# Kernel optimization log

Hardware: AMD Instinct MI355X
Metric: run time of the kernel (lower is better)

Reference implementation:

```python
import jax, jax.numpy as jnp
import numpy as np

DIM_V = 1024
NUM_HEADS = 64            # per the module arg name; actually the per-chunk size
DIM_SPLIT = DIM_V // NUM_HEADS  # 16 = effective number of attention heads (module quirk)
N_Q, N_K = 2048, 2048
DIM_Q, DIM_K = 1024, 1024


def setup_inputs() -> dict:
    key = jax.random.key(0)
    ks = jax.random.split(key, 10)
    s = 0.02
    return {
        "Q": jax.random.normal(ks[0], (N_Q, DIM_Q), dtype=jnp.float32),
        "K": jax.random.normal(ks[1], (N_K, DIM_K), dtype=jnp.float32),
        "Wq": jax.random.normal(ks[2], (DIM_V, DIM_Q), dtype=jnp.float32) * s,
        "bq": jax.random.normal(ks[3], (DIM_V,), dtype=jnp.float32) * s,
        "Wk": jax.random.normal(ks[4], (DIM_V, DIM_K), dtype=jnp.float32) * s,
        "bk": jax.random.normal(ks[5], (DIM_V,), dtype=jnp.float32) * s,
        "Wv": jax.random.normal(ks[6], (DIM_V, DIM_K), dtype=jnp.float32) * s,
        "bv": jax.random.normal(ks[7], (DIM_V,), dtype=jnp.float32) * s,
        "Wo": jax.random.normal(ks[8], (DIM_V, DIM_V), dtype=jnp.float32) * s,
        "bo": jax.random.normal(ks[9], (DIM_V,), dtype=jnp.float32) * s,
    }


def _split_heads(x):
    # jnp.split(x[None], DIM_SPLIT, axis=2) then concat on axis 0 ==
    # [DIM_SPLIT, n, NUM_HEADS] with chunk h = x[:, h*NUM_HEADS:(h+1)*NUM_HEADS]
    n = x.shape[0]
    return x.reshape(n, DIM_SPLIT, NUM_HEADS).transpose(1, 0, 2)


def reference(Q, K, Wq, bq, Wk, bk, Wv, bv, Wo, bo):
    q = Q @ Wq.T + bq            # [n_q, dim_V]
    k = K @ Wk.T + bk            # [n_k, dim_V]
    v = K @ Wv.T + bv            # [n_k, dim_V]
    Q_ = _split_heads(q)         # [H, n_q, d] with H=DIM_SPLIT, d=NUM_HEADS
    K_ = _split_heads(k)
    V_ = _split_heads(v)
    # Faithful to source: softmax first, THEN divide by sqrt(dim_V)
    A = jax.nn.softmax(jnp.einsum('hqd,hkd->hqk', Q_, K_), axis=-1)
    A = A / jnp.sqrt(jnp.float32(DIM_V))
    O = (Q_ + jnp.einsum('hqk,hkd->hqd', A, V_)).reshape(-1, DIM_V)  # [n_q, dim_V]
    # res1 = identity (ln=False)
    O = O + jax.nn.relu(O @ Wo.T + bo)
    # res2 = identity (ln=False)
    return O
```

## Files before the change

### kernel.cpp

```cpp
#include <hip/hip_runtime.h>
#include <hip/hip_bf16.h>
#include <cstdint>

typedef unsigned short u16;
typedef __attribute__((ext_vector_type(8))) short short8;
typedef __attribute__((ext_vector_type(4))) float f32x4;

__device__ __forceinline__ u16 f2b(float f) {
  uint32_t u = __float_as_uint(f);
  u += 0x7fffu + ((u >> 16) & 1u);
  return (u16)(u >> 16);
}
__device__ __forceinline__ float b2f(u16 b) {
  return __uint_as_float(((uint32_t)b) << 16);
}
__device__ __forceinline__ uint32_t pk2bf(float a, float b) {
  __hip_bfloat162 t = __float22bfloat162_rn(make_float2(a, b));
  return *(uint32_t*)&t;
}

__global__ __launch_bounds__(256) void cast_all(
    const float* __restrict__ Q, const float* __restrict__ K,
    const float* __restrict__ Wq, const float* __restrict__ Wk,
    const float* __restrict__ Wv, const float* __restrict__ Wo,
    u16* __restrict__ xq, u16* __restrict__ xk,
    u16* __restrict__ wq, u16* __restrict__ wk,
    u16* __restrict__ wv, u16* __restrict__ wo) {
  int g = blockIdx.x * 256 + threadIdx.x;
  const float* src; u16* dst; int off;
  if      (g <  524288) { src = Q;  dst = xq; off = g; }
  else if (g < 1048576) { src = K;  dst = xk; off = g -  524288; }
  else if (g < 1310720) { src = Wq; dst = wq; off = g - 1048576; }
  else if (g < 1572864) { src = Wk; dst = wk; off = g - 1310720; }
  else if (g < 1835008) { src = Wv; dst = wv; off = g - 1572864; }
  else                  { src = Wo; dst = wo; off = g - 1835008; }
  float4 v = reinterpret_cast<const float4*>(src)[off];
  ushort4 o4;
  o4.x = f2b(v.x); o4.y = f2b(v.y); o4.z = f2b(v.z); o4.w = f2b(v.w);
  reinterpret_cast<ushort4*>(dst)[off] = o4;
}

__global__ __launch_bounds__(256) void gemm3(
    const u16* __restrict__ xq, const u16* __restrict__ xk,
    const u16* __restrict__ wq, const u16* __restrict__ wk,
    const u16* __restrict__ wv,
    const float* __restrict__ bq, const float* __restrict__ bk,
    const float* __restrict__ bv,
    u16* __restrict__ qb, u16* __restrict__ kb, u16* __restrict__ vT) {
  __shared__ __align__(16) u16 sA[128 * 40];
  __shared__ __align__(16) u16 sB[64 * 40];
  const int t = threadIdx.x, blk = blockIdx.x, z = blockIdx.y;
  const int xcd = blk & 7, lid = blk >> 3;
  const u16 *A, *B; const float* bias; u16* C; int ldC, mbase, nbase; bool brow;
  if (z == 0)      { A = xq; B = wq; bias = bq; C = qb; ldC = 1024;
                     mbase = (xcd * 2 + (lid >> 4)) * 128; nbase = (lid & 15) * 64; brow = false; }
  else if (z == 1) { A = xk; B = wk; bias = bk; C = kb; ldC = 1024;
                     mbase = (xcd * 2 + (lid >> 4)) * 128; nbase = (lid & 15) * 64; brow = false; }
  else             { A = wv; B = xk; bias = bv; C = vT; ldC = 2048;
                     mbase = xcd * 128; nbase = lid * 64; brow = true; }
  const int lane = t & 63, wid = t >> 6;
  const int wy = wid >> 1, wx = wid & 1;
  const int m = lane & 15, quad = lane >> 4;

  const int arow = t >> 1, acb = (t & 1) * 16;
  const int brow_ = t >> 2, bcb = (t & 3) * 8;
  const u16* gA = A + (mbase + arow) * 1024 + acb;
  const u16* gB = B + (nbase + brow_) * 1024 + bcb;

  uint4 ra0 = *(const uint4*)(gA);
  uint4 ra1 = *(const uint4*)(gA + 8);
  uint4 rb0 = *(const uint4*)(gB);

  f32x4 acc[4][2];
#pragma unroll
  for (int i = 0; i < 4; i++)
#pragma unroll
    for (int j = 0; j < 2; j++) acc[i][j] = (f32x4){0.f, 0.f, 0.f, 0.f};

  for (int kb_ = 0; kb_ < 32; ++kb_) {
    __syncthreads();
    *(uint4*)(&sA[arow * 40 + acb])     = ra0;
    *(uint4*)(&sA[arow * 40 + acb + 8]) = ra1;
    *(uint4*)(&sB[brow_ * 40 + bcb])    = rb0;
    if (kb_ < 31) {
      ra0 = *(const uint4*)(gA + (kb_ + 1) * 32);
      ra1 = *(const uint4*)(gA + (kb_ + 1) * 32 + 8);
      rb0 = *(const uint4*)(gB + (kb_ + 1) * 32);
    }
    __syncthreads();
    short8 af[4], bf[2];
#pragma unroll
    for (int mi = 0; mi < 4; mi++)
      af[mi] = *(const short8*)(&sA[(wy * 64 + mi * 16 + m) * 40 + quad * 8]);
#pragma unroll
    for (int ni = 0; ni < 2; ni++)
      bf[ni] = *(const short8*)(&sB[(wx * 32 + ni * 16 + m) * 40 + quad * 8]);
#pragma unroll
    for (int mi = 0; mi < 4; mi++)
#pragma unroll
      for (int ni = 0; ni < 2; ni++)
        acc[mi][ni] = __builtin_amdgcn_mfma_f32_16x16x32_bf16(
            af[mi], bf[ni], acc[mi][ni], 0, 0, 0);
  }

#pragma unroll
  for (int mi = 0; mi < 4; mi++)
#pragma unroll
    for (int ni = 0; ni < 2; ni++) {
      const int col = nbase + wx * 32 + ni * 16 + m;
      const float bcol = brow ? 0.f : bias[col];
#pragma unroll
      for (int r = 0; r < 4; r++) {
        const int row = mbase + wy * 64 + mi * 16 + quad * 4 + r;
        const float bval = brow ? bias[row] : bcol;
        C[row * ldC + col] = f2b(acc[mi][ni][r] + bval);
      }
    }
}

__global__ __launch_bounds__(256) void gemm_out(
    const u16* __restrict__ A, const u16* __restrict__ B,
    const float* __restrict__ bias, const u16* __restrict__ Res,
    float* __restrict__ out) {
  __shared__ __align__(16) u16 sA[64 * 40];
  __shared__ __align__(16) u16 sB[64 * 40];
  const int t = threadIdx.x, blk = blockIdx.x;
  const int xcd = blk & 7, lid = blk >> 3;
  const int mbase = (xcd * 4 + (lid >> 4)) * 64, nbase = (lid & 15) * 64;
  const int lane = t & 63, wid = t >> 6;
  const int wy = wid >> 1, wx = wid & 1;
  const int m = lane & 15, quad = lane >> 4;
  const int srow = t >> 2, scb = (t & 3) * 8;
  const u16* gA = A + (mbase + srow) * 1024 + scb;
  const u16* gB = B + (nbase + srow) * 1024 + scb;
  uint4 ra = *(const uint4*)gA;
  uint4 rb = *(const uint4*)gB;

  f32x4 acc[2][2];
#pragma unroll
  for (int i = 0; i < 2; i++)
#pragma unroll
    for (int j = 0; j < 2; j++) acc[i][j] = (f32x4){0.f, 0.f, 0.f, 0.f};

  for (int kb_ = 0; kb_ < 32; ++kb_) {
    __syncthreads();
    *(uint4*)(&sA[srow * 40 + scb]) = ra;
    *(uint4*)(&sB[srow * 40 + scb]) = rb;
    if (kb_ < 31) {
      ra = *(const uint4*)(gA + (kb_ + 1) * 32);
      rb = *(const uint4*)(gB + (kb_ + 1) * 32);
    }
    __syncthreads();
    short8 af[2], bf[2];
#pragma unroll
    for (int mi = 0; mi < 2; mi++)
      af[mi] = *(const short8*)(&sA[(wy * 32 + mi * 16 + m) * 40 + quad * 8]);
#pragma unroll
    for (int ni = 0; ni < 2; ni++)
      bf[ni] = *(const short8*)(&sB[(wx * 32 + ni * 16 + m) * 40 + quad * 8]);
#pragma unroll
    for (int mi = 0; mi < 2; mi++)
#pragma unroll
      for (int ni = 0; ni < 2; ni++)
        acc[mi][ni] = __builtin_amdgcn_mfma_f32_16x16x32_bf16(
            af[mi], bf[ni], acc[mi][ni], 0, 0, 0);
  }

#pragma unroll
  for (int mi = 0; mi < 2; mi++)
#pragma unroll
    for (int ni = 0; ni < 2; ni++) {
      const int col = nbase + wx * 32 + ni * 16 + m;
      const float bcol = bias[col];
#pragma unroll
      for (int r = 0; r < 4; r++) {
        const int row = mbase + wy * 32 + mi * 16 + quad * 4 + r;
        out[row * 1024 + col] =
            b2f(Res[row * 1024 + col]) + fmaxf(acc[mi][ni][r] + bcol, 0.f);
      }
    }
}

__global__ __launch_bounds__(256, 2) void flash(
    const u16* __restrict__ q, const u16* __restrict__ k,
    const u16* __restrict__ vT, u16* __restrict__ po, float* __restrict__ lp) {
  __shared__ __align__(16) u16 sK[64 * 72];
  __shared__ __align__(16) u16 sV[64 * 72];
  __shared__ __align__(16) u16 sP[4 * 64 * 72];
  const int t = threadIdx.x;
  const int qt = blockIdx.x, h = blockIdx.y, sp = blockIdx.z;
  const int lane = t & 63, wid = t >> 6;
  const int m = lane & 15, quad = lane >> 4;
  const int colbase = h * 64;
  const int pbase = wid * 4608;
  const int kbase = sp * 512;
  const int qwave = qt * 256 + wid * 64;

  short8 aq[4][2];
#pragma unroll
  for (int mi = 0; mi < 4; mi++)
#pragma unroll
    for (int g = 0; g < 2; g++)
      aq[mi][g] = *(const short8*)(
          &q[(qwave + mi * 16 + m) * 1024 + colbase + g * 32 + quad * 8]);

  f32x4 o[4][4];
  float lpart[4] = {0.f, 0.f, 0.f, 0.f};
#pragma unroll
  for (int mi = 0; mi < 4; mi++)
#pragma unroll
    for (int nt = 0; nt < 4; nt++) o[mi][nt] = (f32x4){0.f, 0.f, 0.f, 0.f};

  const int srow = t >> 2, scb = (t & 3) * 16;
  const u16* gK = k + (kbase + srow) * 1024 + colbase + scb;
  const u16* gV = vT + (colbase + srow) * 2048 + kbase + scb;

  uint4 rk0 = *(const uint4*)(gK), rk1 = *(const uint4*)(gK + 8);
  uint4 rv0 = *(const uint4*)(gV), rv1 = *(const uint4*)(gV + 8);

  uint32_t* sP32 = (uint32_t*)sP;

  for (int kt = 0; kt < 8; ++kt) {
    __syncthreads();
    *(uint4*)(&sK[srow * 72 + scb])     = rk0;
    *(uint4*)(&sK[srow * 72 + scb + 8]) = rk1;
    *(uint4*)(&sV[srow * 72 + scb])     = rv0;
    *(uint4*)(&sV[srow * 72 + scb + 8]) = rv1;
    if (kt < 7) {
      rk0 = *(const uint4*)(gK + (kt + 1) * 65536);
      rk1 = *(const uint4*)(gK + (kt + 1) * 65536 + 8);
      rv0 = *(const uint4*)(gV + (kt + 1) * 64);
      rv1 = *(const uint4*)(gV + (kt + 1) * 64 + 8);
    }
    __syncthreads();

#pragma unroll
    for (int nt = 0; nt < 4; nt++) {
      short8 bk0 = *(const short8*)(&sK[(nt * 16 + m) * 72 + quad * 8]);
      short8 bk1 = *(const short8*)(&sK[(nt * 16 + m) * 72 + 32 + quad * 8]);
#pragma unroll
      for (int mi = 0; mi < 4; mi++) {
        f32x4 st = (f32x4){0.f, 0.f, 0.f, 0.f};
        st = __builtin_amdgcn_mfma_f32_16x16x32_bf16(bk0, aq[mi][0], st, 0, 0, 0);
        st = __builtin_amdgcn_mfma_f32_16x16x32_bf16(bk1, aq[mi][1], st, 0, 0, 0);
        float p0 = __expf(st[0] - 16.0f);
        float p1 = __expf(st[1] - 16.0f);
        float p2 = __expf(st[2] - 16.0f);
        float p3 = __expf(st[3] - 16.0f);
        lpart[mi] += (p0 + p1) + (p2 + p3);
        const int pa_ = pbase + (mi * 16 + m) * 72 + nt * 16 + quad * 4;
        sP32[pa_ >> 1]       = pk2bf(p0, p1);
        sP32[(pa_ >> 1) + 1] = pk2bf(p2, p3);
      }
    }

    short8 pa[4][2];
#pragma unroll
    for (int mi = 0; mi < 4; mi++)
#pragma unroll
      for (int g = 0; g < 2; g++)
        pa[mi][g] = *(const short8*)(&sP[pbase + (mi * 16 + m) * 72 + g * 32 + quad * 8]);
#pragma unroll
    for (int nt = 0; nt < 4; nt++) {
      short8 bv0 = *(const short8*)(&sV[(nt * 16 + m) * 72 + quad * 8]);
      short8 bv1 = *(const short8*)(&sV[(nt * 16 + m) * 72 + 32 + quad * 8]);
#pragma unroll
      for (int mi = 0; mi < 4; mi++) {
        o[mi][nt] = __builtin_amdgcn_mfma_f32_16x16x32_bf16(pa[mi][0], bv0, o[mi][nt], 0, 0, 0);
        o[mi][nt] = __builtin_amdgcn_mfma_f32_16x16x32_bf16(pa[mi][1], bv1, o[mi][nt], 0, 0, 0);
      }
    }
  }

#pragma unroll
  for (int mi = 0; mi < 4; mi++) {
    float l = lpart[mi];
    l += __shfl_xor(l, 16);
    l += __shfl_xor(l, 32);
    if (quad == 0)
      lp[(sp * 16 + h) * 2048 + qwave + mi * 16 + m] = l;
  }

#pragma unroll
  for (int mi = 0; mi < 4; mi++)
#pragma unroll
    for (int r = 0; r < 4; r++) {
      const int qg = qwave + mi * 16 + quad * 4 + r;
      const int base = ((sp * 16 + h) * 2048 + qg) * 64;
#pragma unroll
      for (int nt = 0; nt < 4; nt++)
        po[base + nt * 16 + m] = f2b(o[mi][nt][r]);
    }
}

__global__ __launch_bounds__(256) void combine(
    const u16* __restrict__ po, const float* __restrict__ lp,
    const u16* __restrict__ qb, u16* __restrict__ ob) {
  const int idx = blockIdx.x * 256 + threadIdx.x;
  const int dq = idx & 15, qg = (idx >> 4) & 2047, h = idx >> 15;
  float acc0 = 0.f, acc1 = 0.f, acc2 = 0.f, acc3 = 0.f, l = 0.f;
#pragma unroll
  for (int s = 0; s < 4; s++) {
    const ushort4 p4 = *(const ushort4*)&po[(((s * 16 + h) * 2048 + qg) * 64) + dq * 4];
    acc0 += b2f(p4.x); acc1 += b2f(p4.y); acc2 += b2f(p4.z); acc3 += b2f(p4.w);
    l += lp[(s * 16 + h) * 2048 + qg];
  }
  const float inv = 1.0f / (l * 32.0f);
  const ushort4 q4 = *(const ushort4*)&qb[qg * 1024 + h * 64 + dq * 4];
  ushort4 o4;
  o4.x = f2b(b2f(q4.x) + acc0 * inv);
  o4.y = f2b(b2f(q4.y) + acc1 * inv);
  o4.z = f2b(b2f(q4.z) + acc2 * inv);
  o4.w = f2b(b2f(q4.w) + acc3 * inv);
  *(ushort4*)&ob[(h * 128 + (qg >> 4)) * 1024 + (qg & 15) * 64 + dq * 4] = o4;
}

extern "C" void kernel_launch(void* const* d_in, const int* in_sizes, int n_in,
                              void* d_out, int out_size, void* d_ws, size_t ws_size,
                              hipStream_t stream) {
  const float* Q  = (const float*)d_in[0];
  const float* K  = (const float*)d_in[1];
  const float* Wq = (const float*)d_in[2];
  const float* bq = (const float*)d_in[3];
  const float* Wk = (const float*)d_in[4];
  const float* bk = (const float*)d_in[5];
  const float* Wv = (const float*)d_in[6];
  const float* bv = (const float*)d_in[7];
  const float* Wo = (const float*)d_in[8];
  const float* bo = (const float*)d_in[9];
  float* out = (float*)d_out;

  u16* ws = (u16*)d_ws;
  u16* xq  = ws;
  u16* xk  = xq  + 2097152;
  u16* wqb = xk  + 2097152;
  u16* wkb = wqb + 1048576;
  u16* wvb = wkb + 1048576;
  u16* wob = wvb + 1048576;
  u16* qb  = wob + 1048576;
  u16* kb  = qb  + 2097152;
  u16* vT  = kb  + 2097152;
  u16* ob  = vT  + 2097152;
  u16* po  = ob  + 2097152;
  float* lp = (float*)(po + 8388608);

  cast_all<<<8192, 256, 0, stream>>>(Q, K, Wq, Wk, Wv, Wo, xq, xk, wqb, wkb, wvb, wob);

  gemm3<<<dim3(256, 3), 256, 0, stream>>>(xq, xk, wqb, wkb, wvb, bq, bk, bv, qb, kb, vT);

  flash<<<dim3(8, 16, 4), 256, 0, stream>>>(qb, kb, vT, po, lp);

  combine<<<2048, 256, 0, stream>>>(po, lp, qb, ob);

  gemm_out<<<512, 256, 0, stream>>>(ob, wob, bo, ob, out);
}
```

Baseline: 170.4 us.

## Fuse split-K combine into flash kernel via last-block atomic counter

Removes the separate combine kernel launch. Each flash block increments a per-(query tile, head) counter after writing its partial output. The block that arrives last reduces the four splits, adds the residual Q, and writes the bf16 output. The counters are zeroed inside the cast kernel. This saves one launch and its tail, at the cost of an atomic, threadfences, and a serial reduction tail in the last-arriving blocks, which may also read the partials with less coalescing.

```diff
diff --git a/kernel.cpp b/kernel.cpp
--- a/kernel.cpp
+++ b/kernel.cpp
@@ -25,8 +25,10 @@
     const float* __restrict__ Wv, const float* __restrict__ Wo,
     u16* __restrict__ xq, u16* __restrict__ xk,
     u16* __restrict__ wq, u16* __restrict__ wk,
-    u16* __restrict__ wv, u16* __restrict__ wo) {
+    u16* __restrict__ wv, u16* __restrict__ wo,
+    uint32_t* __restrict__ cnt) {
   int g = blockIdx.x * 256 + threadIdx.x;
+  if (g < 128) cnt[g] = 0;
   const float* src; u16* dst; int off;
   if      (g <  524288) { src = Q;  dst = xq; off = g; }
   else if (g < 1048576) { src = K;  dst = xk; off = g -  524288; }
@@ -183,7 +185,9 @@
 
 __global__ __launch_bounds__(256, 2) void flash(
     const u16* __restrict__ q, const u16* __restrict__ k,
-    const u16* __restrict__ vT, u16* __restrict__ po, float* __restrict__ lp) {
+    const u16* __restrict__ vT, u16* __restrict__ po, float* __restrict__ lp,
+    uint32_t* __restrict__ cnt, const u16* __restrict__ qb,
+    u16* __restrict__ ob) {
   __shared__ __align__(16) u16 sK[64 * 72];
   __shared__ __align__(16) u16 sV[64 * 72];
   __shared__ __align__(16) u16 sP[4 * 64 * 72];
@@ -291,28 +295,38 @@
       for (int nt = 0; nt < 4; nt++)
         po[base + nt * 16 + m] = f2b(o[mi][nt][r]);
     }
-}
-
-__global__ __launch_bounds__(256) void combine(
-    const u16* __restrict__ po, const float* __restrict__ lp,
-    const u16* __restrict__ qb, u16* __restrict__ ob) {
-  const int idx = blockIdx.x * 256 + threadIdx.x;
-  const int dq = idx & 15, qg = (idx >> 4) & 2047, h = idx >> 15;
-  float acc0 = 0.f, acc1 = 0.f, acc2 = 0.f, acc3 = 0.f, l = 0.f;
-#pragma unroll
-  for (int s = 0; s < 4; s++) {
-    const ushort4 p4 = *(const ushort4*)&po[(((s * 16 + h) * 2048 + qg) * 64) + dq * 4];
-    acc0 += b2f(p4.x); acc1 += b2f(p4.y); acc2 += b2f(p4.z); acc3 += b2f(p4.w);
-    l += lp[(s * 16 + h) * 2048 + qg];
-  }
-  const float inv = 1.0f / (l * 32.0f);
-  const ushort4 q4 = *(const ushort4*)&qb[qg * 1024 + h * 64 + dq * 4];
-  ushort4 o4;
-  o4.x = f2b(b2f(q4.x) + acc0 * inv);
-  o4.y = f2b(b2f(q4.y) + acc1 * inv);
-  o4.z = f2b(b2f(q4.z) + acc2 * inv);
-  o4.w = f2b(b2f(q4.w) + acc3 * inv);
-  *(ushort4*)&ob[(h * 128 + (qg >> 4)) * 1024 + (qg & 15) * 64 + dq * 4] = o4;
+
+  __syncthreads();
+  __shared__ uint32_t s_old;
+  if (t == 0) {
+    __threadfence();
+    s_old = atomicAdd(&cnt[qt * 16 + h], 1u);
+  }
+  __syncthreads();
+  if (s_old == 3u) {
+    __threadfence();
+    const int dq = (t & 15) * 4;
+#pragma unroll
+    for (int qi = 0; qi < 16; qi++) {
+      const int qg = qt * 256 + (t >> 4) * 16 + qi;
+      float a0 = 0.f, a1 = 0.f, a2 = 0.f, a3 = 0.f, l = 0.f;
+#pragma unroll
+      for (int s = 0; s < 4; s++) {
+        const ushort4 p4 =
+            *(const ushort4*)&po[(((s * 16 + h) * 2048 + qg) * 64) + dq];
+        a0 += b2f(p4.x); a1 += b2f(p4.y); a2 += b2f(p4.z); a3 += b2f(p4.w);
+        l += lp[(s * 16 + h) * 2048 + qg];
+      }
+      const float inv = 1.0f / (l * 32.0f);
+      const ushort4 q4 = *(const ushort4*)&qb[qg * 1024 + h * 64 + dq];
+      ushort4 o4;
+      o4.x = f2b(b2f(q4.x) + a0 * inv);
+      o4.y = f2b(b2f(q4.y) + a1 * inv);
+      o4.z = f2b(b2f(q4.z) + a2 * inv);
+      o4.w = f2b(b2f(q4.w) + a3 * inv);
+      *(ushort4*)&ob[(h * 128 + (qg >> 4)) * 1024 + (qg & 15) * 64 + dq] = o4;
+    }
+  }
 }
 
 extern "C" void kernel_launch(void* const* d_in, const int* in_sizes, int n_in,
@@ -343,14 +357,14 @@
   u16* ob  = vT  + 2097152;
   u16* po  = ob  + 2097152;
   float* lp = (float*)(po + 8388608);
-
-  cast_all<<<8192, 256, 0, stream>>>(Q, K, Wq, Wk, Wv, Wo, xq, xk, wqb, wkb, wvb, wob);
+  uint32_t* cnt = (uint32_t*)(lp + 131072);
+
+  cast_all<<<8192, 256, 0, stream>>>(Q, K, Wq, Wk, Wv, Wo, xq, xk, wqb, wkb,
+                                     wvb, wob, cnt);
 
   gemm3<<<dim3(256, 3), 256, 0, stream>>>(xq, xk, wqb, wkb, wvb, bq, bk, bv, qb, kb, vT);
 
-  flash<<<dim3(8, 16, 4), 256, 0, stream>>>(qb, kb, vT, po, lp);
-
-  combine<<<2048, 256, 0, stream>>>(po, lp, qb, ob);
+  flash<<<dim3(8, 16, 4), 256, 0, stream>>>(qb, kb, vT, po, lp, cnt, qb, ob);
 
   gemm_out<<<512, 256, 0, stream>>>(ob, wob, bo, ob, out);
 }
```

Result: slower. 202.1 us (+18.6%).
